# Optimization experiments

Measured on AMD Instinct MI355X. Metric: run time of the kernel, lower is better.

## Reference

```python
import jax, jax.numpy as jnp
import numpy as np

HID, HEADS, LAYERS, EDIM = 128, 2, 3, 1
HEAD_DIM = HID  # out_channels per head (concat=False -> mean over heads)
N_NODES, N_EDGES = 50000, 500000
LN_EPS = 1e-5


def _layer_norm(x, g, b):
    mu = x.mean(-1, keepdims=True)
    var = ((x - mu) ** 2).mean(-1, keepdims=True)
    return (x - mu) * jax.lax.rsqrt(var + LN_EPS) * g + b


def _transformer_conv(x, src, tgt, edge_attr, Wq, bq, Wk, bk, Wv, bv, We, Wskip, bskip):
    # PyG TransformerConv, concat=False, root_weight=True, lin_edge bias=False
    N = x.shape[0]
    E = src.shape[0]
    q = (x @ Wq + bq).reshape(N, HEADS, HEAD_DIM)
    k = (x @ Wk + bk).reshape(N, HEADS, HEAD_DIM)
    v = (x @ Wv + bv).reshape(N, HEADS, HEAD_DIM)
    e = (edge_attr @ We).reshape(E, HEADS, HEAD_DIM)          # [E,H,C]
    k_j = k[src] + e                                          # gather + edge bias
    q_i = q[tgt]
    alpha = (q_i * k_j).sum(-1) / jnp.sqrt(jnp.asarray(HEAD_DIM, x.dtype))  # [E,H]
    # scatter-softmax over incoming edges of each target node
    m = jax.ops.segment_max(alpha, tgt, num_segments=N)       # [N,H]
    a = jnp.exp(alpha - m[tgt])
    denom = jax.ops.segment_sum(a, tgt, num_segments=N)
    a = a / jnp.where(denom[tgt] > 0, denom[tgt], 1.0)
    msg = (v[src] + e) * a[..., None]                         # [E,H,C]
    out = jax.ops.segment_sum(msg, tgt, num_segments=N)       # [N,H,C]
    out = out.mean(axis=1)                                    # concat=False -> head mean
    return out + x @ Wskip + bskip                            # root/skip connection


def reference(x, edge_index, edge_attr, ln_in_g, ln_in_b,
              Wq, bq, Wk, bk, Wv, bv, We, Wskip, bskip, ln_g, ln_b):
    src, tgt = edge_index[0], edge_index[1]
    x = _layer_norm(x, ln_in_g, ln_in_b)
    for l in range(LAYERS):
        h = _transformer_conv(x, src, tgt, edge_attr,
                              Wq[l], bq[l], Wk[l], bk[l], Wv[l], bv[l],
                              We[l], Wskip[l], bskip[l])
        h = jax.nn.elu(h)
        x = _layer_norm(x + h, ln_g[l], ln_b[l])
    return x


def setup_inputs() -> dict:
    key = jax.random.key(0)
    ks = jax.random.split(key, 12)
    HC = HEADS * HEAD_DIM
    s = 1.0 / np.sqrt(HID)
    inp = {
        "x": jax.random.normal(ks[0], (N_NODES, HID), jnp.float32),
        "edge_index": jax.random.randint(ks[1], (2, N_EDGES), 0, N_NODES, jnp.int64),
        "edge_attr": jax.random.normal(ks[2], (N_EDGES, EDIM), jnp.float32),
        "ln_in_g": jnp.ones((HID,), jnp.float32),
        "ln_in_b": jnp.zeros((HID,), jnp.float32),
        "Wq": jax.random.normal(ks[3], (LAYERS, HID, HC), jnp.float32) * s,
        "bq": jnp.zeros((LAYERS, HC), jnp.float32),
        "Wk": jax.random.normal(ks[4], (LAYERS, HID, HC), jnp.float32) * s,
        "bk": jnp.zeros((LAYERS, HC), jnp.float32),
        "Wv": jax.random.normal(ks[5], (LAYERS, HID, HC), jnp.float32) * s,
        "bv": jnp.zeros((LAYERS, HC), jnp.float32),
        "We": jax.random.normal(ks[6], (LAYERS, EDIM, HC), jnp.float32),
        "Wskip": jax.random.normal(ks[7], (LAYERS, HID, HID), jnp.float32) * s,
        "bskip": jnp.zeros((LAYERS, HID), jnp.float32),
        "ln_g": jnp.ones((LAYERS, HID), jnp.float32),
        "ln_b": jnp.zeros((LAYERS, HID), jnp.float32),
    }
    return inp
```

## Files before the change

kernel.cpp:

```cpp
#include <hip/hip_runtime.h>
#include <math.h>

#define NN 50000
#define NE 500000
#define HIDS 128
#define MCOLS 896
#define NLAYERS 3

typedef __attribute__((ext_vector_type(8))) short short8;
typedef __attribute__((ext_vector_type(4))) float floatx4;
typedef _Float16 half8v __attribute__((ext_vector_type(8)));
typedef _Float16 half2v __attribute__((ext_vector_type(2)));

union H2U { half8v v; half2v h[4]; };

#define BSTR 152

#define LNB   12500
#define CNTB  1954
#define PKWB  1355
#define GEMM_BLOCKS 782

static __device__ __forceinline__ unsigned short f2bf(float f) {
    unsigned u = __float_as_uint(f);
    u += 0x7fffu + ((u >> 16) & 1u);
    return (unsigned short)(u >> 16);
}
static __device__ __forceinline__ unsigned short f2h(float f) {
    union { _Float16 h; unsigned short u; } c;
    c.h = (_Float16)f;
    return c.u;
}
static __device__ __forceinline__ float fexp2(float x) {
    float r;
    asm("v_exp_f32 %0, %1" : "=v"(r) : "v"(x));
    return r;
}
#define DPP_ADD(v, ctrl) \
    v += __int_as_float(__builtin_amdgcn_mov_dpp(__float_as_int(v), ctrl, 0xf, 0xf, true))
static __device__ __forceinline__ float wred16(float v) {
    DPP_ADD(v, 0xB1);
    DPP_ADD(v, 0x4E);
    DPP_ADD(v, 0x124);
    DPP_ADD(v, 0x128);
    return v;
}
static __device__ __forceinline__ float wred64(float v) {
    v += __shfl_xor(v, 1, 64);
    v += __shfl_xor(v, 2, 64);
    v += __shfl_xor(v, 4, 64);
    v += __shfl_xor(v, 8, 64);
    v += __shfl_xor(v, 16, 64);
    v += __shfl_xor(v, 32, 64);
    return v;
}

__global__ __launch_bounds__(256) void eatb_fuseA(const float* __restrict__ x, const float* __restrict__ lg,
                                                  const float* __restrict__ lb, float* __restrict__ xout,
                                                  unsigned short* __restrict__ xb,
                                                  const int* __restrict__ tgt, int* __restrict__ cnt,
                                                  const float* __restrict__ Wq, const float* __restrict__ Wk,
                                                  const float* __restrict__ Wv, const float* __restrict__ Ws,
                                                  const float* __restrict__ bq, const float* __restrict__ bk,
                                                  const float* __restrict__ bv, const float* __restrict__ bs,
                                                  unsigned short* __restrict__ Wt, float* __restrict__ bcat) {
    int bid = blockIdx.x;
    if (bid < LNB) {
        int wid = threadIdx.x >> 6, lane = threadIdx.x & 63;
        int n = bid * 4 + wid;
        if (n >= NN) return;
        float2 v = *(const float2*)(x + (size_t)n * HIDS + 2 * lane);
        float mu = wred64(v.x + v.y) * (1.f / 128.f);
        float cx = v.x - mu, cy = v.y - mu;
        float var = wred64(cx * cx + cy * cy) * (1.f / 128.f);
        float r = rsqrtf(var + 1e-5f);
        float2 g2 = *(const float2*)(lg + 2 * lane);
        float2 b2 = *(const float2*)(lb + 2 * lane);
        float2 o;
        o.x = cx * r * g2.x + b2.x;
        o.y = cy * r * g2.y + b2.y;
        *(float2*)(xout + (size_t)n * HIDS + 2 * lane) = o;
        unsigned pk = (unsigned)f2bf(o.x) | ((unsigned)f2bf(o.y) << 16);
        *(unsigned*)(xb + (size_t)n * HIDS + 2 * lane) = pk;
    } else if (bid < LNB + CNTB) {
        int e = (bid - LNB) * 256 + threadIdx.x;
        if (e < NE) atomicAdd(&cnt[tgt[e]], 1);
    } else {
        const float QS = 0.08838834764831845f * 1.4426950408889634f;
        int idx = (bid - LNB - CNTB) * 256 + threadIdx.x;
        const int WTOT = NLAYERS * MCOLS * HIDS;
        if (idx < WTOT) {
            int l = idx / (MCOLS * HIDS);
            int rem = idx % (MCOLS * HIDS);
            int c = rem / HIDS, k = rem % HIDS;
            float v;
            if (c < 256)      v = Wq[(l * HIDS + k) * 256 + c] * QS;
            else if (c < 512) v = Wk[(l * HIDS + k) * 256 + c - 256];
            else if (c < 768) v = Wv[(l * HIDS + k) * 256 + c - 512];
            else              v = Ws[(l * HIDS + k) * 128 + c - 768];
            Wt[idx] = f2bf(v);
        } else {
            int i2 = idx - WTOT;
            if (i2 < NLAYERS * MCOLS) {
                int l = i2 / MCOLS, c = i2 % MCOLS;
                float v;
                if (c < 256)      v = bq[l * 256 + c] * QS;
                else if (c < 512) v = bk[l * 256 + c - 256];
                else if (c < 768) v = bv[l * 256 + c - 512];
                else              v = bs[l * 128 + c - 768];
                bcat[i2] = v;
            }
        }
    }
}

__global__ __launch_bounds__(256) void eatb_blocksum(const int* __restrict__ cnt, int* __restrict__ bsums) {
    __shared__ int sm[256];
    int i = blockIdx.x * 256 + threadIdx.x;
    sm[threadIdx.x] = (i < NN) ? cnt[i] : 0;
    __syncthreads();
    for (int off = 128; off > 0; off >>= 1) {
        if (threadIdx.x < off) sm[threadIdx.x] += sm[threadIdx.x + off];
        __syncthreads();
    }
    if (threadIdx.x == 0) bsums[blockIdx.x] = sm[0];
}

__global__ __launch_bounds__(256) void eatb_scanb(int* __restrict__ bsums, int nb) {
    __shared__ int sm[256];
    int t = threadIdx.x;
    int v = (t < nb) ? bsums[t] : 0;
    sm[t] = v;
    __syncthreads();
    for (int off = 1; off < 256; off <<= 1) {
        int x = (t >= off) ? sm[t - off] : 0;
        __syncthreads();
        sm[t] += x;
        __syncthreads();
    }
    if (t < nb) bsums[t] = sm[t] - v;
}

__global__ __launch_bounds__(256) void eatb_rowstart(const int* __restrict__ cnt, const int* __restrict__ bsums,
                                                     int* __restrict__ row_start) {
    __shared__ int sm[256];
    int t = threadIdx.x;
    int i = blockIdx.x * 256 + t;
    int v = (i < NN) ? cnt[i] : 0;
    sm[t] = v;
    __syncthreads();
    for (int off = 1; off < 256; off <<= 1) {
        int x = (t >= off) ? sm[t - off] : 0;
        __syncthreads();
        sm[t] += x;
        __syncthreads();
    }
    int excl = sm[t] - v + bsums[blockIdx.x];
    if (i < NN) row_start[i] = excl;
}

static __device__ __forceinline__ void gemm_body(int bid,
                                                 const unsigned short* __restrict__ xb,
                                                 const unsigned short* __restrict__ Wt,
                                                 const float* __restrict__ bias,
                                                 unsigned short* __restrict__ qpack,
                                                 unsigned short* __restrict__ kvpack,
                                                 unsigned short* __restrict__ skipbuf,
                                                 short* Bs, float* Cs) {
    int tid = threadIdx.x;
    int r0 = bid * 64;
    int wid = tid >> 6, lane = tid & 63;
    int fr = lane & 15;
    int kq = (lane >> 4) * 8;

    int ar = r0 + wid * 16 + fr;
    bool aok = ar < NN;
    const unsigned short* aptr = xb + (size_t)(aok ? ar : 0) * HIDS;
    short8 afk[4];
    #pragma unroll
    for (int ks = 0; ks < 4; ++ks) afk[ks] = *(const short8*)(aptr + ks * 32 + kq);
    if (!aok) {
        short8 z = {};
        afk[0] = z; afk[1] = z; afk[2] = z; afk[3] = z;
    }

    int brow = tid >> 4, bch = (tid & 15) * 8;
    #pragma unroll
    for (int p = 0; p < 4; ++p) {
        int r = brow + p * 16;
        *(uint4*)(Bs + r * BSTR + bch) = *(const uint4*)(Wt + (size_t)r * HIDS + bch);
    }
    __syncthreads();

    int cl = (tid & 15) * 4;
    for (int ci = 0; ci < 14; ++ci) {
        floatx4 acc[4] = {};
        #pragma unroll
        for (int ks = 0; ks < 4; ++ks) {
            int kof = ks * 32 + kq;
            #pragma unroll
            for (int n = 0; n < 4; ++n) {
                short8 bf = *(const short8*)(Bs + (n * 16 + fr) * BSTR + kof);
                acc[n] = __builtin_amdgcn_mfma_f32_16x16x32_bf16(afk[ks], bf, acc[n], 0, 0, 0);
            }
        }
        #pragma unroll
        for (int n = 0; n < 4; ++n)
            #pragma unroll
            for (int rg = 0; rg < 4; ++rg)
                Cs[(wid * 16 + (lane >> 4) * 4 + rg) * 68 + n * 16 + fr] = acc[n][rg];
        __syncthreads();

        int c0 = ci * 64;
        int C = c0 + cl;
        float4 b4 = *(const float4*)(bias + C);
        #pragma unroll
        for (int p = 0; p < 4; ++p) {
            int rr = (tid >> 4) + 16 * p;
            int gr = r0 + rr;
            if (gr < NN) {
                float4 cv = *(const float4*)(Cs + rr * 68 + cl);
                ushort4 o;
                o.x = f2h(cv.x + b4.x);
                o.y = f2h(cv.y + b4.y);
                o.z = f2h(cv.z + b4.z);
                o.w = f2h(cv.w + b4.w);
                if (C < 256)      *(ushort4*)(qpack + (size_t)gr * 256 + C) = o;
                else if (C < 768) *(ushort4*)(kvpack + (size_t)gr * 512 + (C - 256)) = o;
                else              *(ushort4*)(skipbuf + (size_t)gr * 128 + (C - 768)) = o;
            }
        }
        if (ci < 13) {
            #pragma unroll
            for (int p = 0; p < 4; ++p) {
                int r = brow + p * 16;
                *(uint4*)(Bs + r * BSTR + bch) = *(const uint4*)(Wt + (size_t)((ci + 1) * 64 + r) * HIDS + bch);
            }
        }
        __syncthreads();
    }
}

__global__ __launch_bounds__(256) void eatb_gemm(const unsigned short* __restrict__ xb,
                                                 const unsigned short* __restrict__ Wt,
                                                 const float* __restrict__ bias,
                                                 unsigned short* __restrict__ qpack,
                                                 unsigned short* __restrict__ kvpack,
                                                 unsigned short* __restrict__ skipbuf) {
    __shared__ __align__(16) short Bs[64 * BSTR];
    __shared__ __align__(16) float Cs[64 * 68];
    gemm_body(blockIdx.x, xb, Wt, bias, qpack, kvpack, skipbuf, Bs, Cs);
}

__global__ __launch_bounds__(256) void eatb_fuseE(const unsigned short* __restrict__ xb,
                                                  const unsigned short* __restrict__ Wt,
                                                  const float* __restrict__ bias,
                                                  unsigned short* __restrict__ qpack,
                                                  unsigned short* __restrict__ kvpack,
                                                  unsigned short* __restrict__ skipbuf,
                                                  const int* __restrict__ src, const int* __restrict__ tgt,
                                                  const float* __restrict__ ea, int* __restrict__ row_state,
                                                  int2* __restrict__ csr) {
    __shared__ __align__(16) short Bs[64 * BSTR];
    __shared__ __align__(16) float Cs[64 * 68];
    int bid = blockIdx.x;
    if (bid < GEMM_BLOCKS) {
        gemm_body(bid, xb, Wt, bias, qpack, kvpack, skipbuf, Bs, Cs);
    } else {
        int e = (bid - GEMM_BLOCKS) * 256 + threadIdx.x;
        if (e >= NE) return;
        int t = tgt[e];
        int pos = atomicAdd(&row_state[t], 1);
        int2 val;
        val.x = src[e];
        val.y = __float_as_int(ea[e]);
        csr[pos] = val;
    }
}

__global__ __launch_bounds__(256) void eatb_attn(const unsigned short* __restrict__ qpack,
                                                 const unsigned short* __restrict__ kvpack,
                                                 const unsigned short* __restrict__ skipbuf,
                                                 const int2* __restrict__ csr, const int* __restrict__ row_state,
                                                 const float* __restrict__ Wel, const float* __restrict__ g,
                                                 const float* __restrict__ beta, const float* __restrict__ xcur,
                                                 float* __restrict__ dst, unsigned short* __restrict__ xbout) {
    int wid = threadIdx.x >> 6;
    int lane = threadIdx.x & 63;
    int n = blockIdx.x * 4 + wid;
    if (n >= NN) return;
    int slot = lane >> 5;
    int h = (lane >> 4) & 1;
    int sl = lane & 15;
    int dbase = sl * 8;

    const _Float16* qh16 = (const _Float16*)qpack;
    const _Float16* kvh = (const _Float16*)kvpack;

    half8v qh = *(const half8v*)(qh16 + n * 256 + h * 128 + dbase);
    H2U qq; qq.v = qh;
    const float* wep = Wel + h * 128 + dbase;
    float qwe;
    {
        float4 wa = *(const float4*)wep;
        float4 wb = *(const float4*)(wep + 4);
        qwe = wred16((float)qh[0] * wa.x + (float)qh[1] * wa.y + (float)qh[2] * wa.z + (float)qh[3] * wa.w +
                     (float)qh[4] * wb.x + (float)qh[5] * wb.y + (float)qh[6] * wb.z + (float)qh[7] * wb.w);
    }

    float s0 = 0.f, s1 = 0.f, sea0 = 0.f, sea1 = 0.f;
    float a0[8] = {0.f, 0.f, 0.f, 0.f, 0.f, 0.f, 0.f, 0.f};
    float a1[8] = {0.f, 0.f, 0.f, 0.f, 0.f, 0.f, 0.f, 0.f};

    int end = row_state[n];
    int beg = (n > 0) ? row_state[n - 1] : 0;
    int nit = (end - beg + 7) >> 3;
    int lbase = (h << 7) + (sl << 3);

    int2 cA, cB, cC, cD;
    if (nit > 0) {
        int e = beg + slot;
        cA = csr[(e < end) ? e : beg];
        cB = csr[(e + 2 < end) ? e + 2 : beg];
        cC = csr[(e + 4 < end) ? e + 4 : beg];
        cD = csr[(e + 6 < end) ? e + 6 : beg];
    }

    for (int it = 0; it < nit; ++it) {
        int ebase = beg + 8 * it + slot;
        bool vA = ebase < end, vB = ebase + 2 < end, vC = ebase + 4 < end, vD = ebase + 6 < end;
        float eaA = __int_as_float(cA.y);
        float eaB = __int_as_float(cB.y);
        float eaC = __int_as_float(cC.y);
        float eaD = __int_as_float(cD.y);
        int koA = (cA.x << 9) + lbase;
        int koB = (cB.x << 9) + lbase;
        int koC = (cC.x << 9) + lbase;
        int koD = (cD.x << 9) + lbase;
        half8v kA = *(const half8v*)(kvh + koA);
        half8v kB = *(const half8v*)(kvh + koB);
        half8v kC = *(const half8v*)(kvh + koC);
        half8v kD = *(const half8v*)(kvh + koD);
        half8v vA8 = *(const half8v*)(kvh + koA + 256);
        half8v vB8 = *(const half8v*)(kvh + koB + 256);
        half8v vC8 = *(const half8v*)(kvh + koC + 256);
        half8v vD8 = *(const half8v*)(kvh + koD + 256);
        __builtin_amdgcn_sched_barrier(0);
        if (it + 1 < nit) {
            int e2 = ebase + 8;
            cA = csr[(e2 < end) ? e2 : beg];
            cB = csr[(e2 + 2 < end) ? e2 + 2 : beg];
            cC = csr[(e2 + 4 < end) ? e2 + 4 : beg];
            cD = csr[(e2 + 6 < end) ? e2 + 6 : beg];
        }

        H2U ka, kb, kc, kd;
        ka.v = kA; kb.v = kB; kc.v = kC; kd.v = kD;
        float dA0 = __builtin_amdgcn_fdot2(qq.h[0], ka.h[0], 0.f, false);
        float dA1 = __builtin_amdgcn_fdot2(qq.h[1], ka.h[1], 0.f, false);
        dA0 = __builtin_amdgcn_fdot2(qq.h[2], ka.h[2], dA0, false);
        dA1 = __builtin_amdgcn_fdot2(qq.h[3], ka.h[3], dA1, false);
        float dB0 = __builtin_amdgcn_fdot2(qq.h[0], kb.h[0], 0.f, false);
        float dB1 = __builtin_amdgcn_fdot2(qq.h[1], kb.h[1], 0.f, false);
        dB0 = __builtin_amdgcn_fdot2(qq.h[2], kb.h[2], dB0, false);
        dB1 = __builtin_amdgcn_fdot2(qq.h[3], kb.h[3], dB1, false);
        float dC0 = __builtin_amdgcn_fdot2(qq.h[0], kc.h[0], 0.f, false);
        float dC1 = __builtin_amdgcn_fdot2(qq.h[1], kc.h[1], 0.f, false);
        dC0 = __builtin_amdgcn_fdot2(qq.h[2], kc.h[2], dC0, false);
        dC1 = __builtin_amdgcn_fdot2(qq.h[3], kc.h[3], dC1, false);
        float dD0 = __builtin_amdgcn_fdot2(qq.h[0], kd.h[0], 0.f, false);
        float dD1 = __builtin_amdgcn_fdot2(qq.h[1], kd.h[1], 0.f, false);
        dD0 = __builtin_amdgcn_fdot2(qq.h[2], kd.h[2], dD0, false);
        dD1 = __builtin_amdgcn_fdot2(qq.h[3], kd.h[3], dD1, false);
        float pA = wred16(dA0 + dA1);
        float pB = wred16(dB0 + dB1);
        float pC = wred16(dC0 + dC1);
        float pD = wred16(dD0 + dD1);
        float wA = vA ? fexp2(fmaf(eaA, qwe, pA)) : 0.f;
        float wB = vB ? fexp2(fmaf(eaB, qwe, pB)) : 0.f;
        float wC = vC ? fexp2(fmaf(eaC, qwe, pC)) : 0.f;
        float wD = vD ? fexp2(fmaf(eaD, qwe, pD)) : 0.f;
        s0 += wA; s1 += wB; s0 += wC; s1 += wD;
        sea0 = fmaf(wA, eaA, sea0);
        sea1 = fmaf(wB, eaB, sea1);
        sea0 = fmaf(wC, eaC, sea0);
        sea1 = fmaf(wD, eaD, sea1);
        #pragma unroll
        for (int d = 0; d < 8; ++d) {
            a0[d] = fmaf(wA, (float)vA8[d], a0[d]);
            a1[d] = fmaf(wB, (float)vB8[d], a1[d]);
            a0[d] = fmaf(wC, (float)vC8[d], a0[d]);
            a1[d] = fmaf(wD, (float)vD8[d], a1[d]);
        }
    }

    float s = s0 + s1, sea = sea0 + sea1;
    float o0 = a0[0] + a1[0], o1 = a0[1] + a1[1], o2 = a0[2] + a1[2], o3 = a0[3] + a1[3];
    float o4 = a0[4] + a1[4], o5 = a0[5] + a1[5], o6 = a0[6] + a1[6], o7 = a0[7] + a1[7];

    s += __shfl_xor(s, 32, 64);
    sea += __shfl_xor(sea, 32, 64);
    o0 += __shfl_xor(o0, 32, 64);
    o1 += __shfl_xor(o1, 32, 64);
    o2 += __shfl_xor(o2, 32, 64);
    o3 += __shfl_xor(o3, 32, 64);
    o4 += __shfl_xor(o4, 32, 64);
    o5 += __shfl_xor(o5, 32, 64);
    o6 += __shfl_xor(o6, 32, 64);
    o7 += __shfl_xor(o7, 32, 64);

    float4 wea = *(const float4*)wep;
    float4 web = *(const float4*)(wep + 4);

    float inv = (s > 0.f) ? 1.f / s : 1.f;
    float sw = sea * inv;
    o0 = o0 * inv + sw * wea.x;
    o1 = o1 * inv + sw * wea.y;
    o2 = o2 * inv + sw * wea.z;
    o3 = o3 * inv + sw * wea.w;
    o4 = o4 * inv + sw * web.x;
    o5 = o5 * inv + sw * web.y;
    o6 = o6 * inv + sw * web.z;
    o7 = o7 * inv + sw * web.w;
    o0 = 0.5f * (o0 + __shfl_xor(o0, 16, 64));
    o1 = 0.5f * (o1 + __shfl_xor(o1, 16, 64));
    o2 = 0.5f * (o2 + __shfl_xor(o2, 16, 64));
    o3 = 0.5f * (o3 + __shfl_xor(o3, 16, 64));
    o4 = 0.5f * (o4 + __shfl_xor(o4, 16, 64));
    o5 = 0.5f * (o5 + __shfl_xor(o5, 16, 64));
    o6 = 0.5f * (o6 + __shfl_xor(o6, 16, 64));
    o7 = 0.5f * (o7 + __shfl_xor(o7, 16, 64));

    const _Float16* skp = (const _Float16*)skipbuf + n * 128 + dbase;
    half8v skh = *(const half8v*)skp;
    const float* xrp = xcur + n * 128 + dbase;
    float4 xra = *(const float4*)xrp, xrb = *(const float4*)(xrp + 4);
    float y0 = o0 + (float)skh[0], y1 = o1 + (float)skh[1], y2 = o2 + (float)skh[2], y3 = o3 + (float)skh[3];
    float y4 = o4 + (float)skh[4], y5 = o5 + (float)skh[5], y6 = o6 + (float)skh[6], y7 = o7 + (float)skh[7];
    y0 = (y0 > 0.f) ? y0 : __expf(y0) - 1.f;
    y1 = (y1 > 0.f) ? y1 : __expf(y1) - 1.f;
    y2 = (y2 > 0.f) ? y2 : __expf(y2) - 1.f;
    y3 = (y3 > 0.f) ? y3 : __expf(y3) - 1.f;
    y4 = (y4 > 0.f) ? y4 : __expf(y4) - 1.f;
    y5 = (y5 > 0.f) ? y5 : __expf(y5) - 1.f;
    y6 = (y6 > 0.f) ? y6 : __expf(y6) - 1.f;
    y7 = (y7 > 0.f) ? y7 : __expf(y7) - 1.f;
    float p0 = xra.x + y0, p1 = xra.y + y1, p2 = xra.z + y2, p3 = xra.w + y3;
    float p4 = xrb.x + y4, p5 = xrb.y + y5, p6 = xrb.z + y6, p7 = xrb.w + y7;
    float mu = wred16(p0 + p1 + p2 + p3 + p4 + p5 + p6 + p7) * (1.f / 128.f);
    float c0 = p0 - mu, c1 = p1 - mu, c2 = p2 - mu, c3 = p3 - mu;
    float c4 = p4 - mu, c5 = p5 - mu, c6 = p6 - mu, c7 = p7 - mu;
    float var = wred16(c0 * c0 + c1 * c1 + c2 * c2 + c3 * c3 +
                       c4 * c4 + c5 * c5 + c6 * c6 + c7 * c7) * (1.f / 128.f);
    float r = rsqrtf(var + 1e-5f);
    if (lane < 16) {
        const float* gp = g + dbase;
        const float* bp = beta + dbase;
        float4 ga = *(const float4*)gp, gb = *(const float4*)(gp + 4);
        float4 ba = *(const float4*)bp, bb = *(const float4*)(bp + 4);
        float4 oa, ob;
        oa.x = c0 * r * ga.x + ba.x; oa.y = c1 * r * ga.y + ba.y;
        oa.z = c2 * r * ga.z + ba.z; oa.w = c3 * r * ga.w + ba.w;
        ob.x = c4 * r * gb.x + bb.x; ob.y = c5 * r * gb.y + bb.y;
        ob.z = c6 * r * gb.z + bb.z; ob.w = c7 * r * gb.w + bb.w;
        float* dp = dst + n * 128 + dbase;
        *(float4*)dp = oa;
        *(float4*)(dp + 4) = ob;
        if (xbout) {
            uint4 pk;
            pk.x = (unsigned)f2bf(oa.x) | ((unsigned)f2bf(oa.y) << 16);
            pk.y = (unsigned)f2bf(oa.z) | ((unsigned)f2bf(oa.w) << 16);
            pk.z = (unsigned)f2bf(ob.x) | ((unsigned)f2bf(ob.y) << 16);
            pk.w = (unsigned)f2bf(ob.z) | ((unsigned)f2bf(ob.w) << 16);
            *(uint4*)(xbout + n * 128 + dbase) = pk;
        }
    }
}

extern "C" void kernel_launch(void* const* d_in, const int* in_sizes, int n_in,
                              void* d_out, int out_size, void* d_ws, size_t ws_size,
                              hipStream_t stream) {
    const float* x       = (const float*)d_in[0];
    const int*   ei      = (const int*)d_in[1];
    const float* eattr   = (const float*)d_in[2];
    const float* ln_in_g = (const float*)d_in[3];
    const float* ln_in_b = (const float*)d_in[4];
    const float* Wq = (const float*)d_in[5];
    const float* bq = (const float*)d_in[6];
    const float* Wk = (const float*)d_in[7];
    const float* bk = (const float*)d_in[8];
    const float* Wv = (const float*)d_in[9];
    const float* bv = (const float*)d_in[10];
    const float* We = (const float*)d_in[11];
    const float* Ws = (const float*)d_in[12];
    const float* bs = (const float*)d_in[13];
    const float* ln_g = (const float*)d_in[14];
    const float* ln_b = (const float*)d_in[15];
    float* out = (float*)d_out;

    char* p = (char*)d_ws;
    auto carve = [&](size_t bytes) {
        char* r = p;
        p += (bytes + 255) & ~(size_t)255;
        return (void*)r;
    };
    int*  cnt       = (int*)carve((size_t)NN * 4);
    int*  row_state = (int*)carve((size_t)NN * 4);
    int*  bsums     = (int*)carve(1024);
    int2* csr       = (int2*)carve((size_t)NE * 8);
    unsigned short* WcatT = (unsigned short*)carve((size_t)NLAYERS * MCOLS * HIDS * 2);
    float* bcat     = (float*)carve((size_t)NLAYERS * MCOLS * 4);
    float* xcur     = (float*)carve((size_t)NN * HIDS * 4);
    unsigned short* qpack  = (unsigned short*)carve((size_t)NN * 256 * 2);
    unsigned short* kvpack = (unsigned short*)carve((size_t)NN * 512 * 2);
    unsigned short* skipbuf = (unsigned short*)carve((size_t)NN * HIDS * 2);
    unsigned short* xb = (unsigned short*)carve((size_t)NN * HIDS * 2);

    const int NB_N = (NN + 255) / 256;
    const int NODE_BLOCKS = (NN + 3) / 4;

    hipMemsetAsync(cnt, 0, (size_t)NN * 4, stream);
    eatb_fuseA<<<LNB + CNTB + PKWB, 256, 0, stream>>>(x, ln_in_g, ln_in_b, xcur, xb,
                                                      ei + NE, cnt,
                                                      Wq, Wk, Wv, Ws, bq, bk, bv, bs, WcatT, bcat);

    eatb_blocksum<<<NB_N, 256, 0, stream>>>(cnt, bsums);
    eatb_scanb<<<1, 256, 0, stream>>>(bsums, NB_N);
    eatb_rowstart<<<NB_N, 256, 0, stream>>>(cnt, bsums, row_state);

    eatb_fuseE<<<GEMM_BLOCKS + CNTB, 256, 0, stream>>>(xb, WcatT, bcat, qpack, kvpack, skipbuf,
                                                       ei, ei + NE, eattr, row_state, csr);

    for (int l = 0; l < NLAYERS; ++l) {
        if (l > 0) {
            eatb_gemm<<<GEMM_BLOCKS, 256, 0, stream>>>(xb, WcatT + (size_t)l * MCOLS * HIDS,
                                                       bcat + (size_t)l * MCOLS, qpack, kvpack, skipbuf);
        }
        float* dst = (l == NLAYERS - 1) ? out : xcur;
        unsigned short* xbo = (l == NLAYERS - 1) ? nullptr : xb;
        eatb_attn<<<NODE_BLOCKS, 256, 0, stream>>>(qpack, kvpack, skipbuf, csr, row_state,
                                                   We + (size_t)l * 256, ln_g + (size_t)l * 128,
                                                   ln_b + (size_t)l * 128, xcur, dst, xbo);
    }
    (void)in_sizes; (void)n_in; (void)out_size; (void)ws_size;
}
```

Before: 501.2 us.

## Retile projection GEMM so each block keeps one weight tile and streams rows

The fused Q/K/V/skip projection GEMM used to give each block 64 rows and loop over all 14 column tiles, reloading the weight tile from global memory into LDS at every step. Now a 2D grid gives each block one 64-column weight tile held in LDS and four 64-row tiles of activations. Bias is added and the result converted to half before the LDS staging, and the staging buffer is half-width and double-buffered so one barrier per step is dropped. In exchange, activation rows are now read 14 times across blocks, where before each weight tile was reread by every block.

```diff
diff --git a/kernel.cpp b/kernel.cpp
--- a/kernel.cpp
+++ b/kernel.cpp
@@ -19,7 +19,9 @@
 #define LNB   12500
 #define CNTB  1954
 #define PKWB  1355
-#define GEMM_BLOCKS 782
+#define NCT   14
+#define NBY   196
+#define GEMM_BLOCKS (NCT * NBY)
 
 static __device__ __forceinline__ unsigned short f2bf(float f) {
     unsigned u = __float_as_uint(f);
@@ -159,85 +161,73 @@
     if (i < NN) row_start[i] = excl;
 }
 
-static __device__ __forceinline__ void gemm_body(int bid,
+static __device__ __forceinline__ void gemm_body(int ct, int by,
                                                  const unsigned short* __restrict__ xb,
                                                  const unsigned short* __restrict__ Wt,
                                                  const float* __restrict__ bias,
                                                  unsigned short* __restrict__ qpack,
                                                  unsigned short* __restrict__ kvpack,
                                                  unsigned short* __restrict__ skipbuf,
-                                                 short* Bs, float* Cs) {
+                                                 short* Bs, unsigned short* Csh) {
     int tid = threadIdx.x;
-    int r0 = bid * 64;
     int wid = tid >> 6, lane = tid & 63;
     int fr = lane & 15;
     int kq = (lane >> 4) * 8;
-
-    int ar = r0 + wid * 16 + fr;
-    bool aok = ar < NN;
-    const unsigned short* aptr = xb + (size_t)(aok ? ar : 0) * HIDS;
-    short8 afk[4];
-    #pragma unroll
-    for (int ks = 0; ks < 4; ++ks) afk[ks] = *(const short8*)(aptr + ks * 32 + kq);
-    if (!aok) {
-        short8 z = {};
-        afk[0] = z; afk[1] = z; afk[2] = z; afk[3] = z;
-    }
 
     int brow = tid >> 4, bch = (tid & 15) * 8;
     #pragma unroll
     for (int p = 0; p < 4; ++p) {
         int r = brow + p * 16;
-        *(uint4*)(Bs + r * BSTR + bch) = *(const uint4*)(Wt + (size_t)r * HIDS + bch);
-    }
+        *(uint4*)(Bs + r * BSTR + bch) = *(const uint4*)(Wt + (size_t)(ct * 64 + r) * HIDS + bch);
+    }
+
+    float bl[4];
+    #pragma unroll
+    for (int n = 0; n < 4; ++n) bl[n] = bias[ct * 64 + n * 16 + fr];
+
+    unsigned short* dstb;
+    int dstride, cbase;
+    if (ct < 4)       { dstb = qpack;   dstride = 256; cbase = ct * 64; }
+    else if (ct < 12) { dstb = kvpack;  dstride = 512; cbase = (ct - 4) * 64; }
+    else              { dstb = skipbuf; dstride = 128; cbase = (ct - 12) * 64; }
+
     __syncthreads();
 
     int cl = (tid & 15) * 4;
-    for (int ci = 0; ci < 14; ++ci) {
+    for (int s = 0; s < 4; ++s) {
+        int r0 = by * 256 + s * 64;
+        int ar = r0 + wid * 16 + fr;
+        bool aok = ar < NN;
+        const unsigned short* aptr = xb + (size_t)(aok ? ar : 0) * HIDS;
+
         floatx4 acc[4] = {};
         #pragma unroll
         for (int ks = 0; ks < 4; ++ks) {
             int kof = ks * 32 + kq;
+            short8 af = *(const short8*)(aptr + kof);
+            if (!aok) { short8 z = {}; af = z; }
             #pragma unroll
             for (int n = 0; n < 4; ++n) {
                 short8 bf = *(const short8*)(Bs + (n * 16 + fr) * BSTR + kof);
-                acc[n] = __builtin_amdgcn_mfma_f32_16x16x32_bf16(afk[ks], bf, acc[n], 0, 0, 0);
+                acc[n] = __builtin_amdgcn_mfma_f32_16x16x32_bf16(af, bf, acc[n], 0, 0, 0);
             }
         }
+        unsigned short* Cb = Csh + (s & 1) * (64 * 68);
         #pragma unroll
         for (int n = 0; n < 4; ++n)
             #pragma unroll
             for (int rg = 0; rg < 4; ++rg)
-                Cs[(wid * 16 + (lane >> 4) * 4 + rg) * 68 + n * 16 + fr] = acc[n][rg];
+                Cb[(wid * 16 + (lane >> 4) * 4 + rg) * 68 + n * 16 + fr] = f2h(acc[n][rg] + bl[n]);
         __syncthreads();
-
-        int c0 = ci * 64;
-        int C = c0 + cl;
-        float4 b4 = *(const float4*)(bias + C);
         #pragma unroll
         for (int p = 0; p < 4; ++p) {
             int rr = (tid >> 4) + 16 * p;
             int gr = r0 + rr;
             if (gr < NN) {
-                float4 cv = *(const float4*)(Cs + rr * 68 + cl);
-                ushort4 o;
-                o.x = f2h(cv.x + b4.x);
-                o.y = f2h(cv.y + b4.y);
-                o.z = f2h(cv.z + b4.z);
-                o.w = f2h(cv.w + b4.w);
-                if (C < 256)      *(ushort4*)(qpack + (size_t)gr * 256 + C) = o;
-                else if (C < 768) *(ushort4*)(kvpack + (size_t)gr * 512 + (C - 256)) = o;
-                else              *(ushort4*)(skipbuf + (size_t)gr * 128 + (C - 768)) = o;
+                ushort4 o = *(const ushort4*)(Cb + rr * 68 + cl);
+                *(ushort4*)(dstb + (size_t)gr * dstride + cbase + cl) = o;
             }
         }
-        if (ci < 13) {
-            #pragma unroll
-            for (int p = 0; p < 4; ++p) {
-                int r = brow + p * 16;
-                *(uint4*)(Bs + r * BSTR + bch) = *(const uint4*)(Wt + (size_t)((ci + 1) * 64 + r) * HIDS + bch);
-            }
-        }
-        __syncthreads();
     }
 }
 
@@ -248,8 +238,8 @@
                                                  unsigned short* __restrict__ kvpack,
                                                  unsigned short* __restrict__ skipbuf) {
     __shared__ __align__(16) short Bs[64 * BSTR];
-    __shared__ __align__(16) float Cs[64 * 68];
-    gemm_body(blockIdx.x, xb, Wt, bias, qpack, kvpack, skipbuf, Bs, Cs);
+    __shared__ __align__(16) unsigned short Csh[2][64 * 68];
+    gemm_body(blockIdx.x, blockIdx.y, xb, Wt, bias, qpack, kvpack, skipbuf, Bs, &Csh[0][0]);
 }
 
 __global__ __launch_bounds__(256) void eatb_fuseE(const unsigned short* __restrict__ xb,
@@ -262,10 +252,10 @@
                                                   const float* __restrict__ ea, int* __restrict__ row_state,
                                                   int2* __restrict__ csr) {
     __shared__ __align__(16) short Bs[64 * BSTR];
-    __shared__ __align__(16) float Cs[64 * 68];
+    __shared__ __align__(16) unsigned short Csh[2][64 * 68];
     int bid = blockIdx.x;
     if (bid < GEMM_BLOCKS) {
-        gemm_body(bid, xb, Wt, bias, qpack, kvpack, skipbuf, Bs, Cs);
+        gemm_body(bid / NBY, bid % NBY, xb, Wt, bias, qpack, kvpack, skipbuf, Bs, &Csh[0][0]);
     } else {
         int e = (bid - GEMM_BLOCKS) * 256 + threadIdx.x;
         if (e >= NE) return;
@@ -533,8 +523,8 @@
 
     for (int l = 0; l < NLAYERS; ++l) {
         if (l > 0) {
-            eatb_gemm<<<GEMM_BLOCKS, 256, 0, stream>>>(xb, WcatT + (size_t)l * MCOLS * HIDS,
-                                                       bcat + (size_t)l * MCOLS, qpack, kvpack, skipbuf);
+            eatb_gemm<<<dim3(NCT, NBY), 256, 0, stream>>>(xb, WcatT + (size_t)l * MCOLS * HIDS,
+                                                          bcat + (size_t)l * MCOLS, qpack, kvpack, skipbuf);
         }
         float* dst = (l == NLAYERS - 1) ? out : xcur;
         unsigned short* xbo = (l == NLAYERS - 1) ? nullptr : xb;
```

New measurement: 504.9 us. Within noise of the previous version (+0.7%).

## Overlap CSR prefix-scan kernels with slices of the layer-0 GEMM

Applied to the files above, without the earlier changes.

The three small scan kernels (block sums, scan of block sums, row starts) become extra blocks inside three kernels that each also run a slice of the layer-0 QKV/skip GEMM (166, 166 and 450 row tiles). The block-sum and top-level scan are merged into a single block that reads padded counts as int4. This hides the serial, low-occupancy scan launches behind GEMM work and removes one launch. The count buffer is padded and zeroed so the vectorized reads stay in bounds.

```diff
diff --git a/kernel.cpp b/kernel.cpp
--- a/kernel.cpp
+++ b/kernel.cpp
@@ -20,6 +20,10 @@
 #define CNTB  1954
 #define PKWB  1355
 #define GEMM_BLOCKS 782
+#define GA 166
+#define GB 166
+#define GC 450
+#define NB_N 196
 
 static __device__ __forceinline__ unsigned short f2bf(float f) {
     unsigned u = __float_as_uint(f);
@@ -114,51 +118,6 @@
     }
 }
 
-__global__ __launch_bounds__(256) void eatb_blocksum(const int* __restrict__ cnt, int* __restrict__ bsums) {
-    __shared__ int sm[256];
-    int i = blockIdx.x * 256 + threadIdx.x;
-    sm[threadIdx.x] = (i < NN) ? cnt[i] : 0;
-    __syncthreads();
-    for (int off = 128; off > 0; off >>= 1) {
-        if (threadIdx.x < off) sm[threadIdx.x] += sm[threadIdx.x + off];
-        __syncthreads();
-    }
-    if (threadIdx.x == 0) bsums[blockIdx.x] = sm[0];
-}
-
-__global__ __launch_bounds__(256) void eatb_scanb(int* __restrict__ bsums, int nb) {
-    __shared__ int sm[256];
-    int t = threadIdx.x;
-    int v = (t < nb) ? bsums[t] : 0;
-    sm[t] = v;
-    __syncthreads();
-    for (int off = 1; off < 256; off <<= 1) {
-        int x = (t >= off) ? sm[t - off] : 0;
-        __syncthreads();
-        sm[t] += x;
-        __syncthreads();
-    }
-    if (t < nb) bsums[t] = sm[t] - v;
-}
-
-__global__ __launch_bounds__(256) void eatb_rowstart(const int* __restrict__ cnt, const int* __restrict__ bsums,
-                                                     int* __restrict__ row_start) {
-    __shared__ int sm[256];
-    int t = threadIdx.x;
-    int i = blockIdx.x * 256 + t;
-    int v = (i < NN) ? cnt[i] : 0;
-    sm[t] = v;
-    __syncthreads();
-    for (int off = 1; off < 256; off <<= 1) {
-        int x = (t >= off) ? sm[t - off] : 0;
-        __syncthreads();
-        sm[t] += x;
-        __syncthreads();
-    }
-    int excl = sm[t] - v + bsums[blockIdx.x];
-    if (i < NN) row_start[i] = excl;
-}
-
 static __device__ __forceinline__ void gemm_body(int bid,
                                                  const unsigned short* __restrict__ xb,
                                                  const unsigned short* __restrict__ Wt,
@@ -241,18 +200,74 @@
     }
 }
 
-__global__ __launch_bounds__(256) void eatb_gemm(const unsigned short* __restrict__ xb,
-                                                 const unsigned short* __restrict__ Wt,
-                                                 const float* __restrict__ bias,
-                                                 unsigned short* __restrict__ qpack,
-                                                 unsigned short* __restrict__ kvpack,
-                                                 unsigned short* __restrict__ skipbuf) {
+__global__ __launch_bounds__(256) void eatb_fuseB(const unsigned short* __restrict__ xb,
+                                                  const unsigned short* __restrict__ Wt,
+                                                  const float* __restrict__ bias,
+                                                  unsigned short* __restrict__ qpack,
+                                                  unsigned short* __restrict__ kvpack,
+                                                  unsigned short* __restrict__ skipbuf,
+                                                  const int* __restrict__ cnt, int* __restrict__ bsums) {
     __shared__ __align__(16) short Bs[64 * BSTR];
     __shared__ __align__(16) float Cs[64 * 68];
-    gemm_body(blockIdx.x, xb, Wt, bias, qpack, kvpack, skipbuf, Bs, Cs);
-}
-
-__global__ __launch_bounds__(256) void eatb_fuseE(const unsigned short* __restrict__ xb,
+    int bid = blockIdx.x;
+    if (bid == 0) {
+        int* sm = (int*)Bs;
+        int t = threadIdx.x;
+        int s = 0;
+        if (t < NB_N) {
+            const int4* c4 = (const int4*)cnt;
+            #pragma unroll 4
+            for (int i = 0; i < 64; ++i) {
+                int4 v = c4[t * 64 + i];
+                s += v.x + v.y + v.z + v.w;
+            }
+        }
+        sm[t] = s;
+        __syncthreads();
+        for (int off = 1; off < 256; off <<= 1) {
+            int x = (t >= off) ? sm[t - off] : 0;
+            __syncthreads();
+            sm[t] += x;
+            __syncthreads();
+        }
+        if (t < NB_N) bsums[t] = sm[t] - s;
+    } else {
+        gemm_body(bid - 1, xb, Wt, bias, qpack, kvpack, skipbuf, Bs, Cs);
+    }
+}
+
+__global__ __launch_bounds__(256) void eatb_fuseC(const unsigned short* __restrict__ xb,
+                                                  const unsigned short* __restrict__ Wt,
+                                                  const float* __restrict__ bias,
+                                                  unsigned short* __restrict__ qpack,
+                                                  unsigned short* __restrict__ kvpack,
+                                                  unsigned short* __restrict__ skipbuf,
+                                                  const int* __restrict__ cnt, const int* __restrict__ bsums,
+                                                  int* __restrict__ row_start) {
+    __shared__ __align__(16) short Bs[64 * BSTR];
+    __shared__ __align__(16) float Cs[64 * 68];
+    int bid = blockIdx.x;
+    if (bid < NB_N) {
+        int* sm = (int*)Bs;
+        int t = threadIdx.x;
+        int i = bid * 256 + t;
+        int v = (i < NN) ? cnt[i] : 0;
+        sm[t] = v;
+        __syncthreads();
+        for (int off = 1; off < 256; off <<= 1) {
+            int x = (t >= off) ? sm[t - off] : 0;
+            __syncthreads();
+            sm[t] += x;
+            __syncthreads();
+        }
+        int excl = sm[t] - v + bsums[bid];
+        if (i < NN) row_start[i] = excl;
+    } else {
+        gemm_body(GA + bid - NB_N, xb, Wt, bias, qpack, kvpack, skipbuf, Bs, Cs);
+    }
+}
+
+__global__ __launch_bounds__(256) void eatb_fuseD(const unsigned short* __restrict__ xb,
                                                   const unsigned short* __restrict__ Wt,
                                                   const float* __restrict__ bias,
                                                   unsigned short* __restrict__ qpack,
@@ -264,10 +279,10 @@
     __shared__ __align__(16) short Bs[64 * BSTR];
     __shared__ __align__(16) float Cs[64 * 68];
     int bid = blockIdx.x;
-    if (bid < GEMM_BLOCKS) {
-        gemm_body(bid, xb, Wt, bias, qpack, kvpack, skipbuf, Bs, Cs);
+    if (bid < GC) {
+        gemm_body(GA + GB + bid, xb, Wt, bias, qpack, kvpack, skipbuf, Bs, Cs);
     } else {
-        int e = (bid - GEMM_BLOCKS) * 256 + threadIdx.x;
+        int e = (bid - GC) * 256 + threadIdx.x;
         if (e >= NE) return;
         int t = tgt[e];
         int pos = atomicAdd(&row_state[t], 1);
@@ -276,6 +291,17 @@
         val.y = __float_as_int(ea[e]);
         csr[pos] = val;
     }
+}
+
+__global__ __launch_bounds__(256) void eatb_gemm(const unsigned short* __restrict__ xb,
+                                                 const unsigned short* __restrict__ Wt,
+                                                 const float* __restrict__ bias,
+                                                 unsigned short* __restrict__ qpack,
+                                                 unsigned short* __restrict__ kvpack,
+                                                 unsigned short* __restrict__ skipbuf) {
+    __shared__ __align__(16) short Bs[64 * BSTR];
+    __shared__ __align__(16) float Cs[64 * 68];
+    gemm_body(blockIdx.x, xb, Wt, bias, qpack, kvpack, skipbuf, Bs, Cs);
 }
 
 __global__ __launch_bounds__(256) void eatb_attn(const unsigned short* __restrict__ qpack,
@@ -504,7 +530,8 @@
         p += (bytes + 255) & ~(size_t)255;
         return (void*)r;
     };
-    int*  cnt       = (int*)carve((size_t)NN * 4);
+    const size_t CNT_PAD = 50176;
+    int*  cnt       = (int*)carve(CNT_PAD * 4);
     int*  row_state = (int*)carve((size_t)NN * 4);
     int*  bsums     = (int*)carve(1024);
     int2* csr       = (int2*)carve((size_t)NE * 8);
@@ -516,20 +543,18 @@
     unsigned short* skipbuf = (unsigned short*)carve((size_t)NN * HIDS * 2);
     unsigned short* xb = (unsigned short*)carve((size_t)NN * HIDS * 2);
 
-    const int NB_N = (NN + 255) / 256;
     const int NODE_BLOCKS = (NN + 3) / 4;
 
-    hipMemsetAsync(cnt, 0, (size_t)NN * 4, stream);
+    hipMemsetAsync(cnt, 0, CNT_PAD * 4, stream);
     eatb_fuseA<<<LNB + CNTB + PKWB, 256, 0, stream>>>(x, ln_in_g, ln_in_b, xcur, xb,
                                                       ei + NE, cnt,
                                                       Wq, Wk, Wv, Ws, bq, bk, bv, bs, WcatT, bcat);
 
-    eatb_blocksum<<<NB_N, 256, 0, stream>>>(cnt, bsums);
-    eatb_scanb<<<1, 256, 0, stream>>>(bsums, NB_N);
-    eatb_rowstart<<<NB_N, 256, 0, stream>>>(cnt, bsums, row_state);
-
-    eatb_fuseE<<<GEMM_BLOCKS + CNTB, 256, 0, stream>>>(xb, WcatT, bcat, qpack, kvpack, skipbuf,
-                                                       ei, ei + NE, eattr, row_state, csr);
+    eatb_fuseB<<<1 + GA, 256, 0, stream>>>(xb, WcatT, bcat, qpack, kvpack, skipbuf, cnt, bsums);
+    eatb_fuseC<<<NB_N + GB, 256, 0, stream>>>(xb, WcatT, bcat, qpack, kvpack, skipbuf,
+                                              cnt, bsums, row_state);
+    eatb_fuseD<<<GC + CNTB, 256, 0, stream>>>(xb, WcatT, bcat, qpack, kvpack, skipbuf,
+                                              ei, ei + NE, eattr, row_state, csr);
 
     for (int l = 0; l < NLAYERS; ++l) {
         if (l > 0) {
```

New measurement: 545.4 us. +8.8%, slower.

## Sort nodes into degree buckets so attention waves process similar-degree nodes

Applied to the files above, without the earlier changes.

Builds a 16-bucket histogram of node in-degrees during the row-start scan, then computes a permutation that groups nodes by degree bucket in spare blocks of the fused GEMM/CSR kernel. The attention kernel then maps each wavefront to perm[idx] instead of the node index. The goal is to cut load imbalance and divergence, since nodes in a block now have similar edge counts. The cost is an extra indirection, an extra memset and atomics, and node outputs written in scattered order, which reduces write and qpack locality.

```diff
diff --git a/kernel.cpp b/kernel.cpp
--- a/kernel.cpp
+++ b/kernel.cpp
@@ -20,6 +20,7 @@
 #define CNTB  1954
 #define PKWB  1355
 #define GEMM_BLOCKS 782
+#define PERMB 196
 
 static __device__ __forceinline__ unsigned short f2bf(float f) {
     unsigned u = __float_as_uint(f);
@@ -142,9 +143,11 @@
 }
 
 __global__ __launch_bounds__(256) void eatb_rowstart(const int* __restrict__ cnt, const int* __restrict__ bsums,
-                                                     int* __restrict__ row_start) {
+                                                     int* __restrict__ row_start, int* __restrict__ nhist) {
     __shared__ int sm[256];
+    __shared__ int lh[16];
     int t = threadIdx.x;
+    if (t < 16) lh[t] = 0;
     int i = blockIdx.x * 256 + t;
     int v = (i < NN) ? cnt[i] : 0;
     sm[t] = v;
@@ -156,7 +159,14 @@
         __syncthreads();
     }
     int excl = sm[t] - v + bsums[blockIdx.x];
-    if (i < NN) row_start[i] = excl;
+    if (i < NN) {
+        row_start[i] = excl;
+        int b = (v + 7) >> 3;
+        if (b > 15) b = 15;
+        atomicAdd(&lh[b], 1);
+    }
+    __syncthreads();
+    if (t < 16 && lh[t]) atomicAdd(&nhist[t], lh[t]);
 }
 
 static __device__ __forceinline__ void gemm_body(int bid,
@@ -260,13 +270,15 @@
                                                   unsigned short* __restrict__ skipbuf,
                                                   const int* __restrict__ src, const int* __restrict__ tgt,
                                                   const float* __restrict__ ea, int* __restrict__ row_state,
-                                                  int2* __restrict__ csr) {
+                                                  int2* __restrict__ csr,
+                                                  const int* __restrict__ cnt, const int* __restrict__ nhist,
+                                                  int* __restrict__ ncur, int* __restrict__ perm) {
     __shared__ __align__(16) short Bs[64 * BSTR];
     __shared__ __align__(16) float Cs[64 * 68];
     int bid = blockIdx.x;
     if (bid < GEMM_BLOCKS) {
         gemm_body(bid, xb, Wt, bias, qpack, kvpack, skipbuf, Bs, Cs);
-    } else {
+    } else if (bid < GEMM_BLOCKS + CNTB) {
         int e = (bid - GEMM_BLOCKS) * 256 + threadIdx.x;
         if (e >= NE) return;
         int t = tgt[e];
@@ -275,6 +287,17 @@
         val.x = src[e];
         val.y = __float_as_int(ea[e]);
         csr[pos] = val;
+    } else {
+        int idx = (bid - GEMM_BLOCKS - CNTB) * 256 + threadIdx.x;
+        if (idx >= NN) return;
+        int d = cnt[idx];
+        int b = (d + 7) >> 3;
+        if (b > 15) b = 15;
+        int base = 0;
+        #pragma unroll
+        for (int j = 0; j < 16; ++j) base += (j < b) ? nhist[j] : 0;
+        int pos = base + atomicAdd(&ncur[b], 1);
+        perm[pos] = idx;
     }
 }
 
@@ -282,13 +305,15 @@
                                                  const unsigned short* __restrict__ kvpack,
                                                  const unsigned short* __restrict__ skipbuf,
                                                  const int2* __restrict__ csr, const int* __restrict__ row_state,
+                                                 const int* __restrict__ perm,
                                                  const float* __restrict__ Wel, const float* __restrict__ g,
                                                  const float* __restrict__ beta, const float* __restrict__ xcur,
                                                  float* __restrict__ dst, unsigned short* __restrict__ xbout) {
     int wid = threadIdx.x >> 6;
     int lane = threadIdx.x & 63;
-    int n = blockIdx.x * 4 + wid;
-    if (n >= NN) return;
+    int idx = blockIdx.x * 4 + wid;
+    if (idx >= NN) return;
+    int n = perm[idx];
     int slot = lane >> 5;
     int h = (lane >> 4) & 1;
     int sl = lane & 15;
@@ -507,6 +532,9 @@
     int*  cnt       = (int*)carve((size_t)NN * 4);
     int*  row_state = (int*)carve((size_t)NN * 4);
     int*  bsums     = (int*)carve(1024);
+    int*  nhist     = (int*)carve(256);
+    int*  ncur      = nhist + 16;
+    int*  perm      = (int*)carve((size_t)NN * 4);
     int2* csr       = (int2*)carve((size_t)NE * 8);
     unsigned short* WcatT = (unsigned short*)carve((size_t)NLAYERS * MCOLS * HIDS * 2);
     float* bcat     = (float*)carve((size_t)NLAYERS * MCOLS * 4);
@@ -520,16 +548,18 @@
     const int NODE_BLOCKS = (NN + 3) / 4;
 
     hipMemsetAsync(cnt, 0, (size_t)NN * 4, stream);
+    hipMemsetAsync(nhist, 0, 256, stream);
     eatb_fuseA<<<LNB + CNTB + PKWB, 256, 0, stream>>>(x, ln_in_g, ln_in_b, xcur, xb,
                                                       ei + NE, cnt,
                                                       Wq, Wk, Wv, Ws, bq, bk, bv, bs, WcatT, bcat);
 
     eatb_blocksum<<<NB_N, 256, 0, stream>>>(cnt, bsums);
     eatb_scanb<<<1, 256, 0, stream>>>(bsums, NB_N);
-    eatb_rowstart<<<NB_N, 256, 0, stream>>>(cnt, bsums, row_state);
-
-    eatb_fuseE<<<GEMM_BLOCKS + CNTB, 256, 0, stream>>>(xb, WcatT, bcat, qpack, kvpack, skipbuf,
-                                                       ei, ei + NE, eattr, row_state, csr);
+    eatb_rowstart<<<NB_N, 256, 0, stream>>>(cnt, bsums, row_state, nhist);
+
+    eatb_fuseE<<<GEMM_BLOCKS + CNTB + PERMB, 256, 0, stream>>>(xb, WcatT, bcat, qpack, kvpack, skipbuf,
+                                                               ei, ei + NE, eattr, row_state, csr,
+                                                               cnt, nhist, ncur, perm);
 
     for (int l = 0; l < NLAYERS; ++l) {
         if (l > 0) {
@@ -538,7 +568,7 @@
         }
         float* dst = (l == NLAYERS - 1) ? out : xcur;
         unsigned short* xbo = (l == NLAYERS - 1) ? nullptr : xb;
-        eatb_attn<<<NODE_BLOCKS, 256, 0, stream>>>(qpack, kvpack, skipbuf, csr, row_state,
+        eatb_attn<<<NODE_BLOCKS, 256, 0, stream>>>(qpack, kvpack, skipbuf, csr, row_state, perm,
                                                    We + (size_t)l * 256, ln_g + (size_t)l * 128,
                                                    ln_b + (size_t)l * 128, xcur, dst, xbo);
     }
```

Result: slower. 897.2 us (+79.0%).
